# Optimization experiments

Measured on AMD Instinct MI355X. Metric: run time of the kernel, lower is better.

## Reference

```python
import jax, jax.numpy as jnp
import numpy as np

N = 100000      # nodes
E = 1600000     # edges
DIN = 128       # input_dim
DH = 128        # hidden_dim
DOUT = 64       # output_dim
NL = 10         # num_label_layers


def setup_inputs() -> dict:
    key = jax.random.key(0)
    ks = jax.random.split(key, 12)
    x = jax.random.normal(ks[0], (N, DIN), jnp.float32)
    y = jax.random.uniform(ks[1], (N, DOUT), jnp.float32)
    edge_index = jax.random.randint(ks[2], (2, E), 0, N, dtype=jnp.int32)
    s1 = 1.0 / np.sqrt(DIN)
    s2 = 1.0 / np.sqrt(DH)
    s3 = 1.0 / np.sqrt(DOUT)
    sf = 1.0 / np.sqrt(DH + DOUT)
    Wg1 = jax.random.normal(ks[3], (DIN, DH), jnp.float32) * s1
    bg1 = jnp.zeros((DH,), jnp.float32)
    Wg2 = jax.random.normal(ks[4], (DH, DH), jnp.float32) * s2
    bg2 = jnp.zeros((DH,), jnp.float32)
    Wl = jax.random.normal(ks[5], (NL, DOUT, DOUT), jnp.float32) * s3
    bl = jnp.zeros((NL, DOUT), jnp.float32)
    Wf = jax.random.normal(ks[6], (DH + DOUT, DOUT), jnp.float32) * sf
    bf = jnp.zeros((DOUT,), jnp.float32)
    return {"x": x, "y": y, "edge_index": edge_index,
            "Wg1": Wg1, "bg1": bg1, "Wg2": Wg2, "bg2": bg2,
            "Wl": Wl, "bl": bl, "Wf": Wf, "bf": bf}


def _gcn_conv(h, W, b, src, dst, norm):
    # PyG GCNConv: x' = D^-1/2 (A+I) D^-1/2 (X W) + b
    h = h @ W                                   # [N, dout]
    msg = h[src] * norm[:, None]                # gather + scale: [E+N, dout]
    out = jax.ops.segment_sum(msg, dst, num_segments=N)
    return out + b


def reference(x, y, edge_index, Wg1, bg1, Wg2, bg2, Wl, bl, Wf, bf):
    loops = jnp.arange(N, dtype=edge_index.dtype)
    src = jnp.concatenate([edge_index[0], loops])   # with self-loops
    dst = jnp.concatenate([edge_index[1], loops])
    deg = jax.ops.segment_sum(jnp.ones(dst.shape, jnp.float32), dst, num_segments=N)
    dinv = jnp.where(deg > 0, jax.lax.rsqrt(deg), 0.0)
    norm = dinv[src] * dinv[dst]                    # symmetric GCN normalization

    # GCN feature branch (ReLU between, not after last)
    h = jax.nn.relu(_gcn_conv(x, Wg1, bg1, src, dst, norm))
    h = _gcn_conv(h, Wg2, bg2, src, dst, norm)

    # Label propagation branch
    xl = y
    for j in range(NL):
        xl = _gcn_conv(xl, Wl[j], bl[j], src, dst, norm)
        if j != NL - 1:
            xl = jax.nn.relu(xl)

    fused = jnp.concatenate([h, xl], axis=1) @ Wf + bf
    return jax.nn.sigmoid(fused)
```

## Files before the change

kernel.cpp:

```cpp
#include <hip/hip_runtime.h>
#include <math.h>

#define NN 100000
#define NE 1600000
#define NB 782
#define BCAP 3072
#define BKBLK 128
#define BKCHUNK (NE / BKBLK)
#define DBINS 64

typedef unsigned short ushort_t;
typedef unsigned int uint_t;
typedef __attribute__((ext_vector_type(8))) short bf16x8;
typedef __attribute__((ext_vector_type(8))) unsigned short u16x8;
typedef __attribute__((ext_vector_type(4))) float f32x4;

__device__ __forceinline__ ushort_t f2bf(float f) {
  uint_t u = __float_as_uint(f);
  u = (u + 0x7fffu + ((u >> 16) & 1u)) >> 16;
  return (ushort_t)u;
}
__device__ __forceinline__ float bf2f(ushort_t h) {
  return __uint_as_float((uint_t)h << 16);
}


__global__ __launch_bounds__(512) void bucketA_k(const int* __restrict__ src, const int* __restrict__ dst,
                                                 int* __restrict__ bcnt, uint_t* __restrict__ pairs) {
  __shared__ int h[NB];
  const int t = threadIdx.x;
  const int e0 = blockIdx.x * BKCHUNK;
  for (int b = t; b < NB; b += 512) h[b] = 0;
  __syncthreads();
  for (int i = t; i < BKCHUNK; i += 512) atomicAdd(&h[dst[e0 + i] >> 7], 1);
  __syncthreads();
  for (int b = t; b < NB; b += 512) h[b] = atomicAdd(&bcnt[b], h[b]);
  __syncthreads();
  for (int i = t; i < BKCHUNK; i += 512) {
    int s = src[e0 + i], d = dst[e0 + i];
    int b = d >> 7;
    int pos = atomicAdd(&h[b], 1);
    if (pos < BCAP) pairs[b * BCAP + pos] = ((uint_t)s << 7) | (uint_t)(d & 127);
  }
}

__global__ __launch_bounds__(256) void count2_k(const int* __restrict__ bcnt, const uint_t* __restrict__ pairs,
                                                int* __restrict__ cnt) {
  __shared__ int c[128];
  int b = blockIdx.x, t = threadIdx.x;
  if (t < 128) c[t] = 0;
  __syncthreads();
  int n = min(bcnt[b], BCAP);
  for (int i = t; i < n; i += 256) atomicAdd(&c[pairs[b * BCAP + i] & 127], 1);
  __syncthreads();
  if (t < 128) {
    int node = b * 128 + t;
    if (node < NN) cnt[node] = c[t];
  }
}

__global__ __launch_bounds__(256) void dinv_k(const int* __restrict__ cnt, float* __restrict__ dinv) {
  int i = blockIdx.x * 256 + threadIdx.x;
  if (i < NN) dinv[i] = rsqrtf((float)(cnt[i] + 1));
}

__global__ __launch_bounds__(1024) void scan1(const int* __restrict__ cnt, int* __restrict__ rowstart,
                                              int* __restrict__ blocksum) {
  __shared__ int s[1024];
  int t = threadIdx.x;
  int i = blockIdx.x * 1024 + t;
  int v = (i < NN) ? cnt[i] : 0;
  s[t] = v;
  __syncthreads();
  for (int off = 1; off < 1024; off <<= 1) {
    int add = (t >= off) ? s[t - off] : 0;
    __syncthreads();
    s[t] += add;
    __syncthreads();
  }
  if (i < NN) rowstart[i] = s[t] - v;
  if (t == 1023) blocksum[blockIdx.x] = s[1023];
}

__global__ void scan2(int* blocksum, int nb) {
  if (threadIdx.x == 0 && blockIdx.x == 0) {
    int acc = 0;
    for (int b = 0; b < nb; ++b) { int v = blocksum[b]; blocksum[b] = acc; acc += v; }
  }
}

__global__ __launch_bounds__(1024) void scan3(int* __restrict__ rowstart, const int* __restrict__ blocksum) {
  int i = blockIdx.x * 1024 + threadIdx.x;
  if (i < NN) rowstart[i] += blocksum[blockIdx.x];
}

__global__ __launch_bounds__(256) void fill2_k(const int* __restrict__ bcnt, const uint_t* __restrict__ pairs,
                                               const int* __restrict__ rowstart, int* __restrict__ csr) {
  __shared__ int cur[128];
  int b = blockIdx.x, t = threadIdx.x;
  if (t < 128) cur[t] = 0;
  __syncthreads();
  int n = min(bcnt[b], BCAP);
  for (int i = t; i < n; i += 256) {
    uint_t p = pairs[b * BCAP + i];
    int lo = p & 127;
    int pos = rowstart[b * 128 + lo] + atomicAdd(&cur[lo], 1);
    csr[pos] = (int)(p >> 7);
  }
}


__global__ __launch_bounds__(256) void dhist_k(const int* __restrict__ cnt, int* __restrict__ dbin) {
  __shared__ int h[DBINS];
  int t = threadIdx.x;
  if (t < DBINS) h[t] = 0;
  __syncthreads();
  int i = blockIdx.x * 256 + t;
  if (i < NN) atomicAdd(&h[min(cnt[i], DBINS - 1)], 1);
  __syncthreads();
  if (t < DBINS && h[t]) atomicAdd(&dbin[t], h[t]);
}

__global__ void dscan_k(const int* __restrict__ dbin, int* __restrict__ dcur) {
  if (threadIdx.x == 0 && blockIdx.x == 0) {
    int acc = 0;
    for (int b = 0; b < DBINS; ++b) { dcur[b] = acc; acc += dbin[b]; }
  }
}

__global__ __launch_bounds__(256) void dplace_k(const int* __restrict__ cnt, int* __restrict__ dcur,
                                                int* __restrict__ perm) {
  __shared__ int h[DBINS];
  __shared__ int lbase[DBINS];
  int t = threadIdx.x;
  if (t < DBINS) h[t] = 0;
  __syncthreads();
  int i = blockIdx.x * 256 + t;
  int bin = 0, lrank = 0;
  if (i < NN) { bin = min(cnt[i], DBINS - 1); lrank = atomicAdd(&h[bin], 1); }
  __syncthreads();
  if (t < DBINS) lbase[t] = h[t] ? atomicAdd(&dcur[t], h[t]) : 0;
  __syncthreads();
  if (i < NN) perm[lbase[bin] + lrank] = i;
}


__global__ __launch_bounds__(256) void wprep_k(const float* __restrict__ Wg1, const float* __restrict__ Wl,
                                               ushort_t* __restrict__ G1h, ushort_t* __restrict__ G1l,
                                               ushort_t* __restrict__ Lh, ushort_t* __restrict__ Ll) {
  int i = blockIdx.x * 256 + threadIdx.x;
  if (i >= 57344) return;
  float w;
  ushort_t *ph, *pl;
  size_t di;
  if (i < 16384) {
    int k = i >> 7, n = i & 127;
    w = Wg1[i]; di = (size_t)n * 128 + k; ph = G1h; pl = G1l;
  } else {
    int i2 = i - 16384;
    int j = i2 >> 12, r = i2 & 4095;
    int k = r >> 6, n = r & 63;
    w = Wl[i2]; di = (size_t)j * 4096 + n * 64 + k; ph = Lh; pl = Ll;
  }
  ushort_t h = f2bf(w);
  ph[di] = h;
  pl[di] = f2bf(w - bf2f(h));
}


__global__ __launch_bounds__(256) void ccomp_k(const float* __restrict__ W2, const float* __restrict__ W9,
                                               const float* __restrict__ Wf, const float* __restrict__ b2,
                                               const float* __restrict__ b9, const float* __restrict__ bfb,
                                               ushort_t* __restrict__ Fh, ushort_t* __restrict__ Fl,
                                               float* __restrict__ bc) {
  int i = blockIdx.x * 256 + threadIdx.x;
  if (i >= 12288) return;
  int k = i >> 6, n = i & 63;
  float acc = 0.0f;
  if (k < 128) {
    for (int j = 0; j < 128; ++j) acc += W2[k * 128 + j] * Wf[j * 64 + n];
  } else {
    int k2 = k - 128;
    for (int j = 0; j < 64; ++j) acc += W9[k2 * 64 + j] * Wf[(128 + j) * 64 + n];
  }
  ushort_t h = f2bf(acc);
  Fh[(size_t)n * 192 + k] = h;
  Fl[(size_t)n * 192 + k] = f2bf(acc - bf2f(h));
  if (k == 0) {
    float b = bfb[n];
    for (int j = 0; j < 128; ++j) b += b2[j] * Wf[j * 64 + n];
    for (int j = 0; j < 64; ++j) b += b9[j] * Wf[(128 + j) * 64 + n];
    bc[n] = b;
  }
}


template <int K1, int K2, int DC, bool AF32>
__global__ __launch_bounds__(256) void mgemm_k(const void* __restrict__ A1v, const void* __restrict__ A2v,
                                               const ushort_t* __restrict__ Wth, const ushort_t* __restrict__ Wtl,
                                               const float* __restrict__ dinv, ushort_t* __restrict__ C) {
  constexpr int K = K1 + K2;
  constexpr int NCH = K / 64;
  __shared__ ushort_t Ah[64 * 64];
  __shared__ ushort_t Al[AF32 ? 64 * 64 : 64];
  __shared__ ushort_t Wh[DC * 64], Wl_[DC * 64];
  const int t = threadIdx.x;
  const int row0 = blockIdx.x * 64;
  const int w = t >> 6, l = t & 63;
  const int lr = l & 15, kh = l >> 4;

  f32x4 acc[DC / 16];
  const f32x4 zz = {0.f, 0.f, 0.f, 0.f};
#pragma unroll
  for (int ct = 0; ct < DC / 16; ++ct) acc[ct] = zz;

  for (int kc = 0; kc < NCH; ++kc) {
    if (kc) __syncthreads();
    if constexpr (AF32) {
#pragma unroll
      for (int it = 0; it < 4; ++it) {
        int idx = t + it * 256;
        int row = idx >> 4, kq = idx & 15;
        int gr = min(row0 + row, NN - 1);
        int kbase = kc * 64 + kq * 4;
        float4 a;
        if (K2 > 0 && kbase >= K1)
          a = *(const float4*)&((const float*)A2v)[(size_t)gr * K2 + kbase - K1];
        else
          a = *(const float4*)&((const float*)A1v)[(size_t)gr * K1 + kbase];
        ushort4 h, lo;
        h.x = f2bf(a.x); lo.x = f2bf(a.x - bf2f(h.x));
        h.y = f2bf(a.y); lo.y = f2bf(a.y - bf2f(h.y));
        h.z = f2bf(a.z); lo.z = f2bf(a.z - bf2f(h.z));
        h.w = f2bf(a.w); lo.w = f2bf(a.w - bf2f(h.w));
        int byt = (row * 128 + kq * 8) ^ ((row & 7) << 4);
        *(ushort4*)&Ah[byt >> 1] = h;
        *(ushort4*)&Al[byt >> 1] = lo;
      }
    } else {
#pragma unroll
      for (int it = 0; it < 2; ++it) {
        int idx = t + it * 256;
        int row = idx >> 3, kq = idx & 7;
        int gr = min(row0 + row, NN - 1);
        int kbase = kc * 64 + kq * 8;
        u16x8 v;
        if (K2 > 0 && kbase >= K1)
          v = *(const u16x8*)&((const ushort_t*)A2v)[(size_t)gr * K2 + kbase - K1];
        else
          v = *(const u16x8*)&((const ushort_t*)A1v)[(size_t)gr * K1 + kbase];
        int byt = (row * 128 + kq * 16) ^ ((row & 7) << 4);
        *(u16x8*)&Ah[byt >> 1] = v;
      }
    }
    for (int idx = t; idx < DC * 8; idx += 256) {
      int n = idx >> 3, kq = idx & 7;
      u16x8 hv = *(const u16x8*)&Wth[(size_t)n * K + kc * 64 + kq * 8];
      u16x8 lv = *(const u16x8*)&Wtl[(size_t)n * K + kc * 64 + kq * 8];
      int byt = (n * 128 + kq * 16) ^ ((n & 7) << 4);
      *(u16x8*)&Wh[byt >> 1] = hv;
      *(u16x8*)&Wl_[byt >> 1] = lv;
    }
    __syncthreads();
#pragma unroll
    for (int kc2 = 0; kc2 < 2; ++kc2) {
      int arow = w * 16 + lr;
      int ab = (arow * 128 + kc2 * 64 + kh * 16) ^ ((arow & 7) << 4);
      bf16x8 ah = *(const bf16x8*)&Ah[ab >> 1];
      bf16x8 al;
      if constexpr (AF32) al = *(const bf16x8*)&Al[ab >> 1];
#pragma unroll
      for (int ct = 0; ct < DC / 16; ++ct) {
        int n = ct * 16 + lr;
        int bb = (n * 128 + kc2 * 64 + kh * 16) ^ ((n & 7) << 4);
        bf16x8 bh = *(const bf16x8*)&Wh[bb >> 1];
        bf16x8 bl = *(const bf16x8*)&Wl_[bb >> 1];
        if constexpr (AF32) acc[ct] = __builtin_amdgcn_mfma_f32_16x16x32_bf16(al, bh, acc[ct], 0, 0, 0);
        acc[ct] = __builtin_amdgcn_mfma_f32_16x16x32_bf16(ah, bl, acc[ct], 0, 0, 0);
        acc[ct] = __builtin_amdgcn_mfma_f32_16x16x32_bf16(ah, bh, acc[ct], 0, 0, 0);
      }
    }
  }
  float dv[4];
#pragma unroll
  for (int r = 0; r < 4; ++r) {
    int grow = row0 + w * 16 + kh * 4 + r;
    dv[r] = (grow < NN) ? dinv[grow] : 0.0f;
  }
#pragma unroll
  for (int ct = 0; ct < DC / 16; ++ct) {
    int col = ct * 16 + lr;
#pragma unroll
    for (int r = 0; r < 4; ++r) {
      int grow = row0 + w * 16 + kh * 4 + r;
      if (grow < NN) C[(size_t)grow * DC + col] = f2bf(acc[ct][r] * dv[r]);
    }
  }
}


template <int D, int MODE>
__global__ __launch_bounds__(256) void agg_k(const uint4* __restrict__ t, const int* __restrict__ perm,
                                             const int* __restrict__ rowstart, const int* __restrict__ cnt,
                                             const int* __restrict__ csr, const float* __restrict__ dinv,
                                             const float* __restrict__ bias, void* __restrict__ outv) {
  constexpr int LPN = D / 8;
  int slot = blockIdx.x * (256 / LPN) + threadIdx.x / LPN;
  int lane = threadIdx.x % LPN;
  if (slot >= NN) return;
  int node = perm[slot];

  float acc[8];
  uint4 sv = t[(size_t)node * LPN + lane];
  {
    uint_t u[4] = {sv.x, sv.y, sv.z, sv.w};
#pragma unroll
    for (int q = 0; q < 4; ++q) {
      acc[2 * q]     = __uint_as_float(u[q] << 16);
      acc[2 * q + 1] = __uint_as_float(u[q] & 0xffff0000u);
    }
  }
  int s = rowstart[node], c = cnt[node];
  int j = 0;
  for (; j + 8 <= c; j += 8) {
    int idx[8];
#pragma unroll
    for (int u = 0; u < 8; ++u) idx[u] = csr[s + j + u];
    uint4 v[8];
#pragma unroll
    for (int u = 0; u < 8; ++u) v[u] = t[(size_t)idx[u] * LPN + lane];
#pragma unroll
    for (int u = 0; u < 8; ++u) {
      uint_t q0 = v[u].x, q1 = v[u].y, q2 = v[u].z, q3 = v[u].w;
      acc[0] += __uint_as_float(q0 << 16); acc[1] += __uint_as_float(q0 & 0xffff0000u);
      acc[2] += __uint_as_float(q1 << 16); acc[3] += __uint_as_float(q1 & 0xffff0000u);
      acc[4] += __uint_as_float(q2 << 16); acc[5] += __uint_as_float(q2 & 0xffff0000u);
      acc[6] += __uint_as_float(q3 << 16); acc[7] += __uint_as_float(q3 & 0xffff0000u);
    }
  }
  for (; j < c; ++j) {
    int sn = csr[s + j];
    uint4 v = t[(size_t)sn * LPN + lane];
    uint_t q0 = v.x, q1 = v.y, q2 = v.z, q3 = v.w;
    acc[0] += __uint_as_float(q0 << 16); acc[1] += __uint_as_float(q0 & 0xffff0000u);
    acc[2] += __uint_as_float(q1 << 16); acc[3] += __uint_as_float(q1 & 0xffff0000u);
    acc[4] += __uint_as_float(q2 << 16); acc[5] += __uint_as_float(q2 & 0xffff0000u);
    acc[6] += __uint_as_float(q3 << 16); acc[7] += __uint_as_float(q3 & 0xffff0000u);
  }
  float dv = dinv[node];
  if constexpr (MODE == 0) {
    u16x8 ov;
#pragma unroll
    for (int q = 0; q < 8; ++q) {
      float o = fmaxf(acc[q] * dv + bias[lane * 8 + q], 0.0f);
      ov[q] = f2bf(o);
    }
    *(u16x8*)&((ushort_t*)outv)[(size_t)node * D + lane * 8] = ov;
  } else {
    float o[8];
#pragma unroll
    for (int q = 0; q < 8; ++q) {
      float v2 = acc[q] * dv + bias[lane * 8 + q];
      o[q] = 1.0f / (1.0f + __expf(-v2));
    }
    float4 o0 = {o[0], o[1], o[2], o[3]};
    float4 o1 = {o[4], o[5], o[6], o[7]};
    float* outf = (float*)outv;
    *(float4*)&outf[(size_t)node * D + lane * 8] = o0;
    *(float4*)&outf[(size_t)node * D + lane * 8 + 4] = o1;
  }
}


extern "C" void kernel_launch(void* const* d_in, const int* in_sizes, int n_in,
                              void* d_out, int out_size, void* d_ws, size_t ws_size,
                              hipStream_t stream) {
  const float* x  = (const float*)d_in[0];
  const float* y  = (const float*)d_in[1];
  const int* ei   = (const int*)d_in[2];
  const float* Wg1 = (const float*)d_in[3];
  const float* bg1 = (const float*)d_in[4];
  const float* Wg2 = (const float*)d_in[5];
  const float* bg2 = (const float*)d_in[6];
  const float* Wl  = (const float*)d_in[7];
  const float* bl  = (const float*)d_in[8];
  const float* Wf  = (const float*)d_in[9];
  const float* bf  = (const float*)d_in[10];
  float* out = (float*)d_out;

  char* ws = (char*)d_ws;
  size_t off = 0;
  auto alloc = [&](size_t bytes) { void* p = ws + off; off += (bytes + 511) & ~(size_t)511; return p; };
  int* cnt      = (int*)alloc((size_t)NN * 4);
  int* rowstart = (int*)alloc((size_t)NN * 4);
  int* blocksum = (int*)alloc(512);
  float* dinv   = (float*)alloc((size_t)NN * 4);
  int* csr      = (int*)alloc((size_t)NE * 4);
  int* bcnt     = (int*)alloc((size_t)NB * 4);
  uint_t* pairs = (uint_t*)alloc((size_t)NB * BCAP * 4);
  int* perm     = (int*)alloc((size_t)NN * 4);
  int* dbin     = (int*)alloc(DBINS * 4);
  int* dcur     = (int*)alloc(DBINS * 4);
  ushort_t* Tb  = (ushort_t*)alloc((size_t)NN * 128 * 2);
  ushort_t* H   = (ushort_t*)alloc((size_t)NN * 128 * 2);
  ushort_t* Ub  = (ushort_t*)alloc((size_t)NN * 64 * 2);
  ushort_t* G1h = (ushort_t*)alloc(128 * 128 * 2);
  ushort_t* G1l = (ushort_t*)alloc(128 * 128 * 2);
  ushort_t* Lh  = (ushort_t*)alloc(10 * 64 * 64 * 2);
  ushort_t* Ll  = (ushort_t*)alloc(10 * 64 * 64 * 2);
  ushort_t* Fh  = (ushort_t*)alloc(64 * 192 * 2);
  ushort_t* Fl  = (ushort_t*)alloc(64 * 192 * 2);
  float* bc     = (float*)alloc(64 * 4);
  ushort_t* xlA = Tb;
  ushort_t* xlB = Tb + (size_t)NN * 64;

  const int* esrc = ei;
  const int* edst = ei + NE;

  wprep_k<<<224, 256, 0, stream>>>(Wg1, Wl, G1h, G1l, Lh, Ll);
  ccomp_k<<<48, 256, 0, stream>>>(Wg2, Wl + (size_t)9 * 4096, Wf, bg2, bl + (size_t)9 * 64, bf, Fh, Fl, bc);
  hipMemsetAsync(bcnt, 0, (size_t)NB * 4, stream);
  hipMemsetAsync(dbin, 0, DBINS * 4, stream);
  bucketA_k<<<BKBLK, 512, 0, stream>>>(esrc, edst, bcnt, pairs);
  count2_k<<<NB, 256, 0, stream>>>(bcnt, pairs, cnt);
  dinv_k<<<(NN + 255) / 256, 256, 0, stream>>>(cnt, dinv);
  scan1<<<98, 1024, 0, stream>>>(cnt, rowstart, blocksum);
  scan2<<<1, 1, 0, stream>>>(blocksum, 98);
  scan3<<<98, 1024, 0, stream>>>(rowstart, blocksum);
  fill2_k<<<NB, 256, 0, stream>>>(bcnt, pairs, rowstart, csr);
  dhist_k<<<(NN + 255) / 256, 256, 0, stream>>>(cnt, dbin);
  dscan_k<<<1, 64, 0, stream>>>(dbin, dcur);
  dplace_k<<<(NN + 255) / 256, 256, 0, stream>>>(cnt, dcur, perm);

  const int GG = (NN + 63) / 64;

  mgemm_k<128, 0, 128, true><<<GG, 256, 0, stream>>>(x, nullptr, G1h, G1l, dinv, Tb);
  agg_k<128, 0><<<NN / 16, 256, 0, stream>>>((const uint4*)Tb, perm, rowstart, cnt, csr, dinv, bg1, H);

  const void* in = y;
  for (int j = 0; j < 9; ++j) {
    ushort_t* nxt = (j & 1) ? xlB : xlA;
    if (j == 0)
      mgemm_k<64, 0, 64, true><<<GG, 256, 0, stream>>>(in, nullptr, Lh, Ll, dinv, Ub);
    else
      mgemm_k<64, 0, 64, false><<<GG, 256, 0, stream>>>(in, nullptr, Lh + (size_t)j * 4096, Ll + (size_t)j * 4096, dinv, Ub);
    agg_k<64, 0><<<NN / 32, 256, 0, stream>>>((const uint4*)Ub, perm, rowstart, cnt, csr, dinv, bl + (size_t)j * 64, nxt);
    in = nxt;
  }

  mgemm_k<128, 64, 64, false><<<GG, 256, 0, stream>>>(H, xlA, Fh, Fl, dinv, Ub);
  agg_k<64, 1><<<NN / 32, 256, 0, stream>>>((const uint4*)Ub, perm, rowstart, cnt, csr, dinv, bc, out);
}
```

Baseline: 690.9 us.

## Load GEMM operands directly from global memory and reverse aggregation node order

The dense GEMM kernel no longer stages A and W tiles through shared memory with barriers. Each lane now loads its MFMA fragments straight from global memory (W through cache) in a fully unrolled K loop. This removes LDS traffic and synchronisation, at the cost of redundant global or L2 reads of the weight tiles across waves. Separately, the aggregation kernel walks the degree-sorted permutation in reverse order, which changes load balance and scheduling.

```diff
diff --git a/kernel.cpp b/kernel.cpp
--- a/kernel.cpp
+++ b/kernel.cpp
@@ -200,87 +200,53 @@
                                                const ushort_t* __restrict__ Wth, const ushort_t* __restrict__ Wtl,
                                                const float* __restrict__ dinv, ushort_t* __restrict__ C) {
   constexpr int K = K1 + K2;
-  constexpr int NCH = K / 64;
-  __shared__ ushort_t Ah[64 * 64];
-  __shared__ ushort_t Al[AF32 ? 64 * 64 : 64];
-  __shared__ ushort_t Wh[DC * 64], Wl_[DC * 64];
   const int t = threadIdx.x;
-  const int row0 = blockIdx.x * 64;
   const int w = t >> 6, l = t & 63;
   const int lr = l & 15, kh = l >> 4;
+  const int row0 = blockIdx.x * 64;
+  const int arow = min(row0 + w * 16 + lr, NN - 1);
 
   f32x4 acc[DC / 16];
   const f32x4 zz = {0.f, 0.f, 0.f, 0.f};
 #pragma unroll
   for (int ct = 0; ct < DC / 16; ++ct) acc[ct] = zz;
 
-  for (int kc = 0; kc < NCH; ++kc) {
-    if (kc) __syncthreads();
+#pragma unroll
+  for (int kc = 0; kc < K / 32; ++kc) {
+    const int kbase = kc * 32 + kh * 8;
+    bf16x8 ah, al;
     if constexpr (AF32) {
-#pragma unroll
-      for (int it = 0; it < 4; ++it) {
-        int idx = t + it * 256;
-        int row = idx >> 4, kq = idx & 15;
-        int gr = min(row0 + row, NN - 1);
-        int kbase = kc * 64 + kq * 4;
-        float4 a;
-        if (K2 > 0 && kbase >= K1)
-          a = *(const float4*)&((const float*)A2v)[(size_t)gr * K2 + kbase - K1];
-        else
-          a = *(const float4*)&((const float*)A1v)[(size_t)gr * K1 + kbase];
-        ushort4 h, lo;
-        h.x = f2bf(a.x); lo.x = f2bf(a.x - bf2f(h.x));
-        h.y = f2bf(a.y); lo.y = f2bf(a.y - bf2f(h.y));
-        h.z = f2bf(a.z); lo.z = f2bf(a.z - bf2f(h.z));
-        h.w = f2bf(a.w); lo.w = f2bf(a.w - bf2f(h.w));
-        int byt = (row * 128 + kq * 8) ^ ((row & 7) << 4);
-        *(ushort4*)&Ah[byt >> 1] = h;
-        *(ushort4*)&Al[byt >> 1] = lo;
+      const float* Ap;
+      if (K2 > 0 && kbase >= K1) Ap = &((const float*)A2v)[(size_t)arow * K2 + kbase - K1];
+      else                       Ap = &((const float*)A1v)[(size_t)arow * K1 + kbase];
+      float4 a0 = *(const float4*)Ap;
+      float4 a1 = *(const float4*)(Ap + 4);
+      float av[8] = {a0.x, a0.y, a0.z, a0.w, a1.x, a1.y, a1.z, a1.w};
+      u16x8 hv, lv;
+#pragma unroll
+      for (int e = 0; e < 8; ++e) {
+        ushort_t h = f2bf(av[e]);
+        hv[e] = h;
+        lv[e] = f2bf(av[e] - bf2f(h));
       }
+      ah = (bf16x8)hv; al = (bf16x8)lv;
     } else {
-#pragma unroll
-      for (int it = 0; it < 2; ++it) {
-        int idx = t + it * 256;
-        int row = idx >> 3, kq = idx & 7;
-        int gr = min(row0 + row, NN - 1);
-        int kbase = kc * 64 + kq * 8;
-        u16x8 v;
-        if (K2 > 0 && kbase >= K1)
-          v = *(const u16x8*)&((const ushort_t*)A2v)[(size_t)gr * K2 + kbase - K1];
-        else
-          v = *(const u16x8*)&((const ushort_t*)A1v)[(size_t)gr * K1 + kbase];
-        int byt = (row * 128 + kq * 16) ^ ((row & 7) << 4);
-        *(u16x8*)&Ah[byt >> 1] = v;
-      }
-    }
-    for (int idx = t; idx < DC * 8; idx += 256) {
-      int n = idx >> 3, kq = idx & 7;
-      u16x8 hv = *(const u16x8*)&Wth[(size_t)n * K + kc * 64 + kq * 8];
-      u16x8 lv = *(const u16x8*)&Wtl[(size_t)n * K + kc * 64 + kq * 8];
-      int byt = (n * 128 + kq * 16) ^ ((n & 7) << 4);
-      *(u16x8*)&Wh[byt >> 1] = hv;
-      *(u16x8*)&Wl_[byt >> 1] = lv;
-    }
-    __syncthreads();
-#pragma unroll
-    for (int kc2 = 0; kc2 < 2; ++kc2) {
-      int arow = w * 16 + lr;
-      int ab = (arow * 128 + kc2 * 64 + kh * 16) ^ ((arow & 7) << 4);
-      bf16x8 ah = *(const bf16x8*)&Ah[ab >> 1];
-      bf16x8 al;
-      if constexpr (AF32) al = *(const bf16x8*)&Al[ab >> 1];
-#pragma unroll
-      for (int ct = 0; ct < DC / 16; ++ct) {
-        int n = ct * 16 + lr;
-        int bb = (n * 128 + kc2 * 64 + kh * 16) ^ ((n & 7) << 4);
-        bf16x8 bh = *(const bf16x8*)&Wh[bb >> 1];
-        bf16x8 bl = *(const bf16x8*)&Wl_[bb >> 1];
-        if constexpr (AF32) acc[ct] = __builtin_amdgcn_mfma_f32_16x16x32_bf16(al, bh, acc[ct], 0, 0, 0);
-        acc[ct] = __builtin_amdgcn_mfma_f32_16x16x32_bf16(ah, bl, acc[ct], 0, 0, 0);
-        acc[ct] = __builtin_amdgcn_mfma_f32_16x16x32_bf16(ah, bh, acc[ct], 0, 0, 0);
-      }
-    }
-  }
+      const ushort_t* Ap;
+      if (K2 > 0 && kbase >= K1) Ap = &((const ushort_t*)A2v)[(size_t)arow * K2 + kbase - K1];
+      else                       Ap = &((const ushort_t*)A1v)[(size_t)arow * K1 + kbase];
+      ah = *(const bf16x8*)Ap;
+    }
+#pragma unroll
+    for (int ct = 0; ct < DC / 16; ++ct) {
+      const int n = ct * 16 + lr;
+      bf16x8 bh = *(const bf16x8*)&Wth[(size_t)n * K + kbase];
+      bf16x8 bl = *(const bf16x8*)&Wtl[(size_t)n * K + kbase];
+      if constexpr (AF32) acc[ct] = __builtin_amdgcn_mfma_f32_16x16x32_bf16(al, bh, acc[ct], 0, 0, 0);
+      acc[ct] = __builtin_amdgcn_mfma_f32_16x16x32_bf16(ah, bl, acc[ct], 0, 0, 0);
+      acc[ct] = __builtin_amdgcn_mfma_f32_16x16x32_bf16(ah, bh, acc[ct], 0, 0, 0);
+    }
+  }
+
   float dv[4];
 #pragma unroll
   for (int r = 0; r < 4; ++r) {
@@ -308,7 +274,7 @@
   int slot = blockIdx.x * (256 / LPN) + threadIdx.x / LPN;
   int lane = threadIdx.x % LPN;
   if (slot >= NN) return;
-  int node = perm[slot];
+  int node = perm[NN - 1 - slot];
 
   float acc[8];
   uint4 sv = t[(size_t)node * LPN + lane];
```

Result: slower. 827.2 us (+19.7%).
